# Optimization experiments

Hardware: AMD Instinct MI355X
Metric: run time of the kernel (lower is better)

The kernel has to match this reference:

```python
import jax, jax.numpy as jnp
import numpy as np

V = 50000
E = 800000
B, CIN, COUT, K = 4, 64, 128, 4


def setup_inputs() -> dict:
    key = jax.random.key(0)
    k1, k2, k3, k4, k5 = jax.random.split(key, 5)
    x = jax.random.normal(k1, (B, CIN, V), dtype=jnp.float32)
    lap_rows = jnp.sort(jax.random.randint(k2, (E,), 0, V, dtype=jnp.int32))
    lap_cols = jax.random.randint(k3, (E,), 0, V, dtype=jnp.int32)
    # scale ~1/sqrt(avg_degree) so recurrence stays bounded (laplacian-like spectrum)
    lap_vals = jax.random.normal(k4, (E,), dtype=jnp.float32) * (1.0 / np.sqrt(16.0))
    # kaiming init per module: std = sqrt(2/(Cin*K))
    weight = jax.random.normal(k5, (K, CIN, COUT), dtype=jnp.float32) * np.sqrt(2.0 / (CIN * K))
    bias = jnp.full((COUT,), 0.01, dtype=jnp.float32)
    return {"x": x, "lap_rows": lap_rows, "lap_cols": lap_cols,
            "lap_vals": lap_vals, "weight": weight, "bias": bias}


def reference(x, lap_rows, lap_cols, lap_vals, weight, bias):
    # x: (B, Cin, V); laplacian sparse COO (rows, cols, vals); weight: (K, Cin, Cout)
    Bn, Cin, Vn = x.shape
    Kn = weight.shape[0]

    def spmm(z):  # z: (V, B*Cin) -> laplacian @ z
        return jax.ops.segment_sum(lap_vals[:, None] * z[lap_cols], lap_rows,
                                   num_segments=Vn)

    def contract(z, w):  # (V, B*Cin) x (Cin, Cout) -> (V, B, Cout)
        return jnp.einsum('vbi,io->vbo', z.reshape(Vn, Bn, Cin), w)

    x0 = jnp.transpose(x, (2, 0, 1)).reshape(Vn, Bn * Cin)
    # fused Chebyshev recurrence: accumulate weight contraction per step
    out = contract(x0, weight[0])
    if Kn > 1:
        x1 = spmm(x0)
        out = out + contract(x1, weight[1])
        for k in range(2, Kn):
            x2 = 2.0 * spmm(x1) - x0
            out = out + contract(x2, weight[k])
            x0, x1 = x1, x2
    out = out + bias  # broadcast over (V, B, Cout)
    return jnp.transpose(out, (1, 2, 0))  # (B, Cout, V)
```

## Files before the change

kernel.cpp:

```cpp
#include <hip/hip_runtime.h>
#include <hip/hip_bf16.h>

#define VN 50000
#define EN 800000
#define BN 4
#define CINN 64
#define COUTN 128
#define KN 4
#define FN 256

typedef __attribute__((ext_vector_type(8))) short short8;
typedef __attribute__((ext_vector_type(8))) unsigned short ushort8;
typedef __attribute__((ext_vector_type(4))) float floatx4;

__device__ __forceinline__ float bf2f(unsigned short u) {
    union { unsigned int i; float f; } c;
    c.i = ((unsigned int)u) << 16;
    return c.f;
}
__device__ __forceinline__ unsigned short f2bf(float f) {
    __hip_bfloat16 h = __float2bfloat16(f);
    return *reinterpret_cast<unsigned short*>(&h);
}

#define RP_BLOCKS 196
#define WT_BLOCKS 128
#define EP_BLOCKS 3125
#define TP_BX 782
#define TP_BLOCKS (TP_BX * 4)

__global__ __launch_bounds__(256) void setup_fused(const int* __restrict__ rows,
                                                   int* __restrict__ row_ptr,
                                                   const float* __restrict__ w,
                                                   ushort* __restrict__ wT,
                                                   const float* __restrict__ x,
                                                   ushort* __restrict__ x0,
                                                   const int* __restrict__ cols,
                                                   const float* __restrict__ vals,
                                                   unsigned long long* __restrict__ epack) {
    __shared__ float tile[64][65];
    int blk = blockIdx.x;
    int tid = threadIdx.x;
    if (blk < RP_BLOCKS) {
        int v = blk * 256 + tid;
        if (v > VN) return;
        int lo = 0, hi = EN;
        while (lo < hi) {
            int mid = (lo + hi) >> 1;
            if (rows[mid] < v) lo = mid + 1; else hi = mid;
        }
        row_ptr[v] = lo;
        return;
    }
    if (blk < RP_BLOCKS + WT_BLOCKS) {
        int idx = (blk - RP_BLOCKS) * 256 + tid;
        int o = idx >> 8;
        int kk = idx & 255;
        wT[idx] = f2bf(w[(size_t)kk * COUTN + o]);
        return;
    }
    if (blk < RP_BLOCKS + WT_BLOCKS + EP_BLOCKS) {
        int idx = (blk - RP_BLOCKS - WT_BLOCKS) * 256 + tid;
        unsigned int c = (unsigned int)cols[idx];
        unsigned int wv = __float_as_uint(vals[idx]);
        epack[idx] = ((unsigned long long)wv << 32) | (unsigned long long)c;
        return;
    }
    int t = blk - RP_BLOCKS - WT_BLOCKS - EP_BLOCKS;
    int v0 = (t % TP_BX) * 64;
    int f0 = (t / TP_BX) * 64;
    int tx = tid & 63;
    int ty = tid >> 6;
#pragma unroll
    for (int r = 0; r < 16; ++r) {
        int f = f0 + ty + r * 4;
        int v = v0 + tx;
        if (v < VN) tile[ty + r * 4][tx] = x[(size_t)f * VN + v];
    }
    __syncthreads();
#pragma unroll
    for (int r = 0; r < 16; ++r) {
        int v = v0 + ty + r * 4;
        int f = f0 + tx;
        if (v < VN) x0[(size_t)v * FN + f] = f2bf(tile[tx][ty + r * 4]);
    }
}

__global__ __launch_bounds__(256) void spmm_cheb_bf16(ushort* __restrict__ out,
                                                      const ushort* __restrict__ z,
                                                      const ushort* __restrict__ prev,
                                                      const int* __restrict__ row_ptr,
                                                      const unsigned long long* __restrict__ epack,
                                                      float alpha, float beta) {
    int row = (int)((blockIdx.x * blockDim.x + threadIdx.x) >> 6);
    int lane = threadIdx.x & 63;
    if (row >= VN) return;
    int e0 = row_ptr[row];
    int e1 = row_ptr[row + 1];
    int half = lane >> 5;
    int fl = (lane & 31) * 8;

    float acc0[8], acc1[8];
#pragma unroll
    for (int j = 0; j < 8; ++j) { acc0[j] = 0.f; acc1[j] = 0.f; }

    int e = e0 + half;
    for (; e + 6 < e1; e += 8) {
        unsigned long long d0 = epack[e];
        unsigned long long d1 = epack[e + 2];
        unsigned long long d2 = epack[e + 4];
        unsigned long long d3 = epack[e + 6];
        ushort8 z0 = *reinterpret_cast<const ushort8*>(z + (size_t)(unsigned int)d0 * FN + fl);
        ushort8 z1 = *reinterpret_cast<const ushort8*>(z + (size_t)(unsigned int)d1 * FN + fl);
        ushort8 z2 = *reinterpret_cast<const ushort8*>(z + (size_t)(unsigned int)d2 * FN + fl);
        ushort8 z3 = *reinterpret_cast<const ushort8*>(z + (size_t)(unsigned int)d3 * FN + fl);
        float w0 = __uint_as_float((unsigned int)(d0 >> 32));
        float w1 = __uint_as_float((unsigned int)(d1 >> 32));
        float w2 = __uint_as_float((unsigned int)(d2 >> 32));
        float w3 = __uint_as_float((unsigned int)(d3 >> 32));
#pragma unroll
        for (int j = 0; j < 8; ++j) acc0[j] += w0 * bf2f(z0[j]);
#pragma unroll
        for (int j = 0; j < 8; ++j) acc1[j] += w1 * bf2f(z1[j]);
#pragma unroll
        for (int j = 0; j < 8; ++j) acc0[j] += w2 * bf2f(z2[j]);
#pragma unroll
        for (int j = 0; j < 8; ++j) acc1[j] += w3 * bf2f(z3[j]);
    }
    for (; e + 2 < e1; e += 4) {
        unsigned long long d0 = epack[e];
        unsigned long long d1 = epack[e + 2];
        ushort8 z0 = *reinterpret_cast<const ushort8*>(z + (size_t)(unsigned int)d0 * FN + fl);
        ushort8 z1 = *reinterpret_cast<const ushort8*>(z + (size_t)(unsigned int)d1 * FN + fl);
        float w0 = __uint_as_float((unsigned int)(d0 >> 32));
        float w1 = __uint_as_float((unsigned int)(d1 >> 32));
#pragma unroll
        for (int j = 0; j < 8; ++j) acc0[j] += w0 * bf2f(z0[j]);
#pragma unroll
        for (int j = 0; j < 8; ++j) acc1[j] += w1 * bf2f(z1[j]);
    }
    for (; e < e1; e += 2) {
        unsigned long long d0 = epack[e];
        ushort8 z0 = *reinterpret_cast<const ushort8*>(z + (size_t)(unsigned int)d0 * FN + fl);
        float w0 = __uint_as_float((unsigned int)(d0 >> 32));
#pragma unroll
        for (int j = 0; j < 8; ++j) acc0[j] += w0 * bf2f(z0[j]);
    }
#pragma unroll
    for (int j = 0; j < 8; ++j) acc0[j] += acc1[j];
#pragma unroll
    for (int j = 0; j < 8; ++j) acc0[j] += __shfl(acc0[j], lane ^ 32);

    if (half == 0) {
        ushort8 res;
        if (beta != 0.f) {
            ushort8 pv = *reinterpret_cast<const ushort8*>(prev + (size_t)row * FN + fl);
#pragma unroll
            for (int j = 0; j < 8; ++j)
                res[j] = f2bf(alpha * acc0[j] + beta * bf2f(pv[j]));
        } else {
#pragma unroll
            for (int j = 0; j < 8; ++j)
                res[j] = f2bf(alpha * acc0[j]);
        }
        *reinterpret_cast<ushort8*>(out + (size_t)row * FN + fl) = res;
    }
}

__global__ __launch_bounds__(256) void cheb_gemm_mfma(float* __restrict__ out,
                                                      const ushort* __restrict__ xbase,
                                                      const ushort* __restrict__ wT,
                                                      const float* __restrict__ bias) {
    __shared__ __align__(16) short lsA[128 * 64];
    __shared__ __align__(16) short lsB[128 * 64];

    int b = blockIdx.y;
    int v0 = blockIdx.x * 128;
    int tid = threadIdx.x;
    int lane = tid & 63;
    int w = tid >> 6;
    int mw = w & 1;
    int nw = w >> 1;
    int ln = lane & 15;
    int quad = lane >> 4;

    int srow = tid >> 1;
    int posBase = (tid & 1) * 4;

    floatx4 acc[4][4];
#pragma unroll
    for (int mi = 0; mi < 4; ++mi)
#pragma unroll
        for (int ni = 0; ni < 4; ++ni) acc[mi][ni] = (floatx4){0.f, 0.f, 0.f, 0.f};

    for (int kc = 0; kc < 4; ++kc) {
        __syncthreads();
#pragma unroll
        for (int j = 0; j < 4; ++j) {
            int pos = posBase + j;
            int g = pos ^ (srow & 7);
            uint4 val = *reinterpret_cast<const uint4*>(wT + (size_t)srow * 256 + kc * 64 + g * 8);
            *reinterpret_cast<uint4*>(&lsA[(srow * 8 + pos) * 8]) = val;
        }
        {
            const ushort* xk = xbase + (size_t)kc * VN * FN;
            int v = v0 + srow;
            bool ok = (v < VN);
            const ushort* src = xk + (size_t)v * FN + b * CINN;
#pragma unroll
            for (int j = 0; j < 4; ++j) {
                int pos = posBase + j;
                int g = pos ^ (srow & 7);
                uint4 val;
                if (ok) val = *reinterpret_cast<const uint4*>(src + g * 8);
                else    val = make_uint4(0u, 0u, 0u, 0u);
                *reinterpret_cast<uint4*>(&lsB[(srow * 8 + pos) * 8]) = val;
            }
        }
        __syncthreads();

#pragma unroll
        for (int s = 0; s < 2; ++s) {
            short8 afr[4], bfr[4];
#pragma unroll
            for (int mi = 0; mi < 4; ++mi) {
                int r = mw * 64 + mi * 16 + ln;
                int pos = (s * 4 + quad) ^ (r & 7);
                afr[mi] = *reinterpret_cast<const short8*>(&lsA[(r * 8 + pos) * 8]);
            }
#pragma unroll
            for (int ni = 0; ni < 4; ++ni) {
                int r = nw * 64 + ni * 16 + ln;
                int pos = (s * 4 + quad) ^ (r & 7);
                bfr[ni] = *reinterpret_cast<const short8*>(&lsB[(r * 8 + pos) * 8]);
            }
#pragma unroll
            for (int mi = 0; mi < 4; ++mi)
#pragma unroll
                for (int ni = 0; ni < 4; ++ni)
                    acc[mi][ni] = __builtin_amdgcn_mfma_f32_16x16x32_bf16(
                        afr[mi], bfr[ni], acc[mi][ni], 0, 0, 0);
        }
    }

#pragma unroll
    for (int mi = 0; mi < 4; ++mi) {
#pragma unroll
        for (int r = 0; r < 4; ++r) {
            int o = mw * 64 + mi * 16 + quad * 4 + r;
            float bv = bias[o];
            size_t obase = (size_t)(b * COUTN + o) * VN;
#pragma unroll
            for (int ni = 0; ni < 4; ++ni) {
                int v = v0 + nw * 64 + ni * 16 + ln;
                if (v < VN) out[obase + v] = acc[mi][ni][r] + bv;
            }
        }
    }
}

extern "C" void kernel_launch(void* const* d_in, const int* in_sizes, int n_in,
                              void* d_out, int out_size, void* d_ws, size_t ws_size,
                              hipStream_t stream) {
    const float* x        = (const float*)d_in[0];
    const int*   lap_rows = (const int*)d_in[1];
    const int*   lap_cols = (const int*)d_in[2];
    const float* lap_vals = (const float*)d_in[3];
    const float* weight   = (const float*)d_in[4];
    const float* bias     = (const float*)d_in[5];
    float* out = (float*)d_out;

    char* ws = (char*)d_ws;
    ushort* x0 = (ushort*)ws;
    ushort* x1 = x0 + (size_t)VN * FN;
    ushort* x2 = x1 + (size_t)VN * FN;
    ushort* x3 = x2 + (size_t)VN * FN;
    size_t xbytes = (size_t)4 * VN * FN * sizeof(ushort);
    int* row_ptr = (int*)(ws + xbytes);
    size_t rp_end = xbytes + (size_t)(VN + 1) * sizeof(int);
    rp_end = (rp_end + 15) & ~(size_t)15;
    ushort* wT = (ushort*)(ws + rp_end);
    size_t wt_end = rp_end + (size_t)COUTN * FN * sizeof(ushort);
    unsigned long long* epack = (unsigned long long*)(ws + wt_end);

    setup_fused<<<RP_BLOCKS + WT_BLOCKS + EP_BLOCKS + TP_BLOCKS, 256, 0, stream>>>(
        lap_rows, row_ptr, weight, wT, x, x0, lap_cols, lap_vals, epack);
    spmm_cheb_bf16<<<(VN + 3) / 4, 256, 0, stream>>>(x1, x0, x0, row_ptr, epack, 1.f, 0.f);
    spmm_cheb_bf16<<<(VN + 3) / 4, 256, 0, stream>>>(x2, x1, x0, row_ptr, epack, 2.f, -1.f);
    spmm_cheb_bf16<<<(VN + 3) / 4, 256, 0, stream>>>(x3, x2, x1, row_ptr, epack, 2.f, -1.f);
    cheb_gemm_mfma<<<dim3((VN + 127) / 128, BN), 256, 0, stream>>>(out, x0, wT, bias);
}
```

Measured before the change: 374.8 us.

## Packed-FMA SpMM accumulation and retiled, prefetched GEMM with vectorized stores

The SpMM inner loops now accumulate in float2 vectors so the compiler can emit packed FMA instructions. The GEMM is retiled to 64 vertices per block, and its operands are swapped so the output fragments run along the vertex dimension. That lets each thread write four contiguous floats per store, and the block now prefetches the next k-chunk into registers before the current chunk's MFMAs run. The aim is lower ALU cost in SpMM and more occupancy, latency hiding and coalesced stores in the GEMM, at the price of more blocks and more loads of the weight tile.

```diff
diff --git a/kernel.cpp b/kernel.cpp
--- a/kernel.cpp
+++ b/kernel.cpp
@@ -12,6 +12,7 @@
 typedef __attribute__((ext_vector_type(8))) short short8;
 typedef __attribute__((ext_vector_type(8))) unsigned short ushort8;
 typedef __attribute__((ext_vector_type(4))) float floatx4;
+typedef __attribute__((ext_vector_type(2))) float floatx2;
 
 __device__ __forceinline__ float bf2f(unsigned short u) {
     union { unsigned int i; float f; } c;
@@ -100,9 +101,11 @@
     int half = lane >> 5;
     int fl = (lane & 31) * 8;
 
-    float acc0[8], acc1[8];
-#pragma unroll
-    for (int j = 0; j < 8; ++j) { acc0[j] = 0.f; acc1[j] = 0.f; }
+    floatx2 A0[4], A1[4];
+#pragma unroll
+    for (int p = 0; p < 4; ++p) { A0[p] = (floatx2){0.f, 0.f}; A1[p] = (floatx2){0.f, 0.f}; }
+
+#define ZPAIR(zz, p) ((floatx2){bf2f((zz)[2*(p)]), bf2f((zz)[2*(p)+1])})
 
     int e = e0 + half;
     for (; e + 6 < e1; e += 8) {
@@ -118,14 +121,16 @@
         float w1 = __uint_as_float((unsigned int)(d1 >> 32));
         float w2 = __uint_as_float((unsigned int)(d2 >> 32));
         float w3 = __uint_as_float((unsigned int)(d3 >> 32));
-#pragma unroll
-        for (int j = 0; j < 8; ++j) acc0[j] += w0 * bf2f(z0[j]);
-#pragma unroll
-        for (int j = 0; j < 8; ++j) acc1[j] += w1 * bf2f(z1[j]);
-#pragma unroll
-        for (int j = 0; j < 8; ++j) acc0[j] += w2 * bf2f(z2[j]);
-#pragma unroll
-        for (int j = 0; j < 8; ++j) acc1[j] += w3 * bf2f(z3[j]);
+        floatx2 wv0 = (floatx2){w0, w0}, wv1 = (floatx2){w1, w1};
+        floatx2 wv2 = (floatx2){w2, w2}, wv3 = (floatx2){w3, w3};
+#pragma unroll
+        for (int p = 0; p < 4; ++p) A0[p] += wv0 * ZPAIR(z0, p);
+#pragma unroll
+        for (int p = 0; p < 4; ++p) A1[p] += wv1 * ZPAIR(z1, p);
+#pragma unroll
+        for (int p = 0; p < 4; ++p) A0[p] += wv2 * ZPAIR(z2, p);
+#pragma unroll
+        for (int p = 0; p < 4; ++p) A1[p] += wv3 * ZPAIR(z3, p);
     }
     for (; e + 2 < e1; e += 4) {
         unsigned long long d0 = epack[e];
@@ -134,20 +139,29 @@
         ushort8 z1 = *reinterpret_cast<const ushort8*>(z + (size_t)(unsigned int)d1 * FN + fl);
         float w0 = __uint_as_float((unsigned int)(d0 >> 32));
         float w1 = __uint_as_float((unsigned int)(d1 >> 32));
-#pragma unroll
-        for (int j = 0; j < 8; ++j) acc0[j] += w0 * bf2f(z0[j]);
-#pragma unroll
-        for (int j = 0; j < 8; ++j) acc1[j] += w1 * bf2f(z1[j]);
+        floatx2 wv0 = (floatx2){w0, w0}, wv1 = (floatx2){w1, w1};
+#pragma unroll
+        for (int p = 0; p < 4; ++p) A0[p] += wv0 * ZPAIR(z0, p);
+#pragma unroll
+        for (int p = 0; p < 4; ++p) A1[p] += wv1 * ZPAIR(z1, p);
     }
     for (; e < e1; e += 2) {
         unsigned long long d0 = epack[e];
         ushort8 z0 = *reinterpret_cast<const ushort8*>(z + (size_t)(unsigned int)d0 * FN + fl);
         float w0 = __uint_as_float((unsigned int)(d0 >> 32));
-#pragma unroll
-        for (int j = 0; j < 8; ++j) acc0[j] += w0 * bf2f(z0[j]);
-    }
-#pragma unroll
-    for (int j = 0; j < 8; ++j) acc0[j] += acc1[j];
+        floatx2 wv0 = (floatx2){w0, w0};
+#pragma unroll
+        for (int p = 0; p < 4; ++p) A0[p] += wv0 * ZPAIR(z0, p);
+    }
+#undef ZPAIR
+
+    float acc0[8];
+#pragma unroll
+    for (int p = 0; p < 4; ++p) {
+        floatx2 m = A0[p] + A1[p];
+        acc0[2 * p] = m[0];
+        acc0[2 * p + 1] = m[1];
+    }
 #pragma unroll
     for (int j = 0; j < 8; ++j) acc0[j] += __shfl(acc0[j], lane ^ 32);
 
@@ -167,93 +181,117 @@
     }
 }
 
-__global__ __launch_bounds__(256) void cheb_gemm_mfma(float* __restrict__ out,
-                                                      const ushort* __restrict__ xbase,
-                                                      const ushort* __restrict__ wT,
-                                                      const float* __restrict__ bias) {
-    __shared__ __align__(16) short lsA[128 * 64];
-    __shared__ __align__(16) short lsB[128 * 64];
+__global__ __launch_bounds__(256, 4) void cheb_gemm_mfma(float* __restrict__ out,
+                                                         const ushort* __restrict__ xbase,
+                                                         const ushort* __restrict__ wT,
+                                                         const float* __restrict__ bias) {
+    __shared__ __align__(16) short lsX[64 * 64];
+    __shared__ __align__(16) short lsW[128 * 64];
 
     int b = blockIdx.y;
-    int v0 = blockIdx.x * 128;
+    int v0 = blockIdx.x * 64;
     int tid = threadIdx.x;
     int lane = tid & 63;
     int w = tid >> 6;
-    int mw = w & 1;
-    int nw = w >> 1;
+    int wv = w & 1;
+    int wo = w >> 1;
     int ln = lane & 15;
     int quad = lane >> 4;
 
-    int srow = tid >> 1;
-    int posBase = (tid & 1) * 4;
-
-    floatx4 acc[4][4];
-#pragma unroll
-    for (int mi = 0; mi < 4; ++mi)
+    int srowW = tid >> 1;
+    int posW0 = (tid & 1) * 4;
+    int srowX = tid >> 2;
+    int posX0 = (tid & 3) * 2;
+    int vX = v0 + srowX;
+    bool okX = (vX < VN);
+
+    floatx4 acc[2][4];
+#pragma unroll
+    for (int mi = 0; mi < 2; ++mi)
 #pragma unroll
         for (int ni = 0; ni < 4; ++ni) acc[mi][ni] = (floatx4){0.f, 0.f, 0.f, 0.f};
 
+    uint4 pW[4], pX[2];
+
+#define LOADW(KC)                                                                       \
+    {                                                                                   \
+        _Pragma("unroll")                                                               \
+        for (int j = 0; j < 4; ++j) {                                                   \
+            int g = (posW0 + j) ^ (srowW & 7);                                          \
+            pW[j] = *reinterpret_cast<const uint4*>(wT + (size_t)srowW * 256 + (KC) * 64 + g * 8); \
+        }                                                                               \
+    }
+#define LOADX(KC)                                                                       \
+    {                                                                                   \
+        const ushort* src = xbase + (size_t)(KC) * VN * FN + (size_t)vX * FN + b * CINN; \
+        _Pragma("unroll")                                                               \
+        for (int j = 0; j < 2; ++j) {                                                   \
+            int g = (posX0 + j) ^ (srowX & 7);                                          \
+            if (okX) pX[j] = *reinterpret_cast<const uint4*>(src + g * 8);              \
+            else     pX[j] = make_uint4(0u, 0u, 0u, 0u);                                \
+        }                                                                               \
+    }
+
+    LOADW(0);
+    LOADX(0);
+
+#pragma unroll
     for (int kc = 0; kc < 4; ++kc) {
         __syncthreads();
 #pragma unroll
-        for (int j = 0; j < 4; ++j) {
-            int pos = posBase + j;
-            int g = pos ^ (srow & 7);
-            uint4 val = *reinterpret_cast<const uint4*>(wT + (size_t)srow * 256 + kc * 64 + g * 8);
-            *reinterpret_cast<uint4*>(&lsA[(srow * 8 + pos) * 8]) = val;
-        }
-        {
-            const ushort* xk = xbase + (size_t)kc * VN * FN;
-            int v = v0 + srow;
-            bool ok = (v < VN);
-            const ushort* src = xk + (size_t)v * FN + b * CINN;
-#pragma unroll
-            for (int j = 0; j < 4; ++j) {
-                int pos = posBase + j;
-                int g = pos ^ (srow & 7);
-                uint4 val;
-                if (ok) val = *reinterpret_cast<const uint4*>(src + g * 8);
-                else    val = make_uint4(0u, 0u, 0u, 0u);
-                *reinterpret_cast<uint4*>(&lsB[(srow * 8 + pos) * 8]) = val;
+        for (int j = 0; j < 4; ++j)
+            *reinterpret_cast<uint4*>(&lsW[(srowW * 8 + posW0 + j) * 8]) = pW[j];
+#pragma unroll
+        for (int j = 0; j < 2; ++j)
+            *reinterpret_cast<uint4*>(&lsX[(srowX * 8 + posX0 + j) * 8]) = pX[j];
+        __syncthreads();
+
+        if (kc < 3) {
+            LOADW(kc + 1);
+            LOADX(kc + 1);
+        }
+
+#pragma unroll
+        for (int s = 0; s < 2; ++s) {
+            short8 afr[2], bfr[4];
+#pragma unroll
+            for (int mi = 0; mi < 2; ++mi) {
+                int r = wv * 32 + mi * 16 + ln;
+                int pos = (s * 4 + quad) ^ (r & 7);
+                afr[mi] = *reinterpret_cast<const short8*>(&lsX[(r * 8 + pos) * 8]);
             }
-        }
-        __syncthreads();
-
-#pragma unroll
-        for (int s = 0; s < 2; ++s) {
-            short8 afr[4], bfr[4];
-#pragma unroll
-            for (int mi = 0; mi < 4; ++mi) {
-                int r = mw * 64 + mi * 16 + ln;
+#pragma unroll
+            for (int ni = 0; ni < 4; ++ni) {
+                int r = wo * 64 + ni * 16 + ln;
                 int pos = (s * 4 + quad) ^ (r & 7);
-                afr[mi] = *reinterpret_cast<const short8*>(&lsA[(r * 8 + pos) * 8]);
+                bfr[ni] = *reinterpret_cast<const short8*>(&lsW[(r * 8 + pos) * 8]);
             }
 #pragma unroll
-            for (int ni = 0; ni < 4; ++ni) {
-                int r = nw * 64 + ni * 16 + ln;
-                int pos = (s * 4 + quad) ^ (r & 7);
-                bfr[ni] = *reinterpret_cast<const short8*>(&lsB[(r * 8 + pos) * 8]);
-            }
-#pragma unroll
-            for (int mi = 0; mi < 4; ++mi)
+            for (int mi = 0; mi < 2; ++mi)
 #pragma unroll
                 for (int ni = 0; ni < 4; ++ni)
                     acc[mi][ni] = __builtin_amdgcn_mfma_f32_16x16x32_bf16(
                         afr[mi], bfr[ni], acc[mi][ni], 0, 0, 0);
         }
     }
-
-#pragma unroll
-    for (int mi = 0; mi < 4; ++mi) {
-#pragma unroll
-        for (int r = 0; r < 4; ++r) {
-            int o = mw * 64 + mi * 16 + quad * 4 + r;
+#undef LOADW
+#undef LOADX
+
+#pragma unroll
+    for (int mi = 0; mi < 2; ++mi) {
+        int vb = v0 + wv * 32 + mi * 16 + quad * 4;
+#pragma unroll
+        for (int ni = 0; ni < 4; ++ni) {
+            int o = wo * 64 + ni * 16 + ln;
             float bv = bias[o];
             size_t obase = (size_t)(b * COUTN + o) * VN;
-#pragma unroll
-            for (int ni = 0; ni < 4; ++ni) {
-                int v = v0 + nw * 64 + ni * 16 + ln;
-                if (v < VN) out[obase + v] = acc[mi][ni][r] + bv;
+            floatx4 res = acc[mi][ni] + bv;
+            if (vb + 3 < VN) {
+                *reinterpret_cast<floatx4*>(out + obase + vb) = res;
+            } else {
+#pragma unroll
+                for (int r = 0; r < 4; ++r)
+                    if (vb + r < VN) out[obase + vb + r] = res[r];
             }
         }
     }
@@ -288,5 +326,5 @@
     spmm_cheb_bf16<<<(VN + 3) / 4, 256, 0, stream>>>(x1, x0, x0, row_ptr, epack, 1.f, 0.f);
     spmm_cheb_bf16<<<(VN + 3) / 4, 256, 0, stream>>>(x2, x1, x0, row_ptr, epack, 2.f, -1.f);
     spmm_cheb_bf16<<<(VN + 3) / 4, 256, 0, stream>>>(x3, x2, x1, row_ptr, epack, 2.f, -1.f);
-    cheb_gemm_mfma<<<dim3((VN + 127) / 128, BN), 256, 0, stream>>>(out, x0, wT, bias);
-}
+    cheb_gemm_mfma<<<dim3((VN + 63) / 64, BN), 256, 0, stream>>>(out, x0, wT, bias);
+}
```

Measured after the change: 421.8 us. 12.5% more time.

## Double-buffer GEMM LDS tiles using direct global-to-LDS async loads

Applied to the files above, without the earlier changes.

Rewrites the Chebyshev GEMM staging so each chunk's weight and feature tiles are loaded with global_load_lds straight into LDS, skipping the trip through registers. Two LDS buffers let the next K-chunk's load overlap the current chunk's MFMA work, with one barrier per iteration instead of two. This doubles LDS use per block to 64KB, which may lower occupancy. It also drops the row bounds check, so the last partial block reads past the valid vertex rows.

```diff
diff --git a/kernel.cpp b/kernel.cpp
--- a/kernel.cpp
+++ b/kernel.cpp
@@ -21,6 +21,12 @@
 __device__ __forceinline__ unsigned short f2bf(float f) {
     __hip_bfloat16 h = __float2bfloat16(f);
     return *reinterpret_cast<unsigned short*>(&h);
+}
+
+typedef __attribute__((address_space(1))) const unsigned int guint;
+typedef __attribute__((address_space(3))) unsigned int luint;
+__device__ __forceinline__ void gload_lds16(const void* g, void* l) {
+    __builtin_amdgcn_global_load_lds((guint*)g, (luint*)l, 16, 0, 0);
 }
 
 #define RP_BLOCKS 196
@@ -171,8 +177,7 @@
                                                       const ushort* __restrict__ xbase,
                                                       const ushort* __restrict__ wT,
                                                       const float* __restrict__ bias) {
-    __shared__ __align__(16) short lsA[128 * 64];
-    __shared__ __align__(16) short lsB[128 * 64];
+    __shared__ __align__(16) short lds[2][16384];
 
     int b = blockIdx.y;
     int v0 = blockIdx.x * 128;
@@ -184,8 +189,8 @@
     int ln = lane & 15;
     int quad = lane >> 4;
 
-    int srow = tid >> 1;
-    int posBase = (tid & 1) * 4;
+    int lr = lane >> 3;
+    int lg = (lane & 7) ^ lr;
 
     floatx4 acc[4][4];
 #pragma unroll
@@ -193,31 +198,26 @@
 #pragma unroll
         for (int ni = 0; ni < 4; ++ni) acc[mi][ni] = (floatx4){0.f, 0.f, 0.f, 0.f};
 
+#define STAGE(BUF, KC)                                                              \
+    {                                                                               \
+        const ushort* xk = xbase + (size_t)(KC) * VN * FN;                          \
+        _Pragma("unroll")                                                           \
+        for (int j = 0; j < 4; ++j) {                                               \
+            int c = w * 4 + j;                                                      \
+            int r = c * 8 + lr;                                                     \
+            gload_lds16(wT + (size_t)r * 256 + (KC) * 64 + lg * 8,                  \
+                        &lds[BUF][c * 512]);                                        \
+            gload_lds16(xk + (size_t)(v0 + r) * FN + b * CINN + lg * 8,             \
+                        &lds[BUF][8192 + c * 512]);                                 \
+        }                                                                           \
+    }
+
+    int cur = 0;
+    STAGE(0, 0);
+    __syncthreads();
+
     for (int kc = 0; kc < 4; ++kc) {
-        __syncthreads();
-#pragma unroll
-        for (int j = 0; j < 4; ++j) {
-            int pos = posBase + j;
-            int g = pos ^ (srow & 7);
-            uint4 val = *reinterpret_cast<const uint4*>(wT + (size_t)srow * 256 + kc * 64 + g * 8);
-            *reinterpret_cast<uint4*>(&lsA[(srow * 8 + pos) * 8]) = val;
-        }
-        {
-            const ushort* xk = xbase + (size_t)kc * VN * FN;
-            int v = v0 + srow;
-            bool ok = (v < VN);
-            const ushort* src = xk + (size_t)v * FN + b * CINN;
-#pragma unroll
-            for (int j = 0; j < 4; ++j) {
-                int pos = posBase + j;
-                int g = pos ^ (srow & 7);
-                uint4 val;
-                if (ok) val = *reinterpret_cast<const uint4*>(src + g * 8);
-                else    val = make_uint4(0u, 0u, 0u, 0u);
-                *reinterpret_cast<uint4*>(&lsB[(srow * 8 + pos) * 8]) = val;
-            }
-        }
-        __syncthreads();
+        if (kc < 3) STAGE(cur ^ 1, kc + 1);
 
 #pragma unroll
         for (int s = 0; s < 2; ++s) {
@@ -226,13 +226,13 @@
             for (int mi = 0; mi < 4; ++mi) {
                 int r = mw * 64 + mi * 16 + ln;
                 int pos = (s * 4 + quad) ^ (r & 7);
-                afr[mi] = *reinterpret_cast<const short8*>(&lsA[(r * 8 + pos) * 8]);
+                afr[mi] = *reinterpret_cast<const short8*>(&lds[cur][(r * 8 + pos) * 8]);
             }
 #pragma unroll
             for (int ni = 0; ni < 4; ++ni) {
                 int r = nw * 64 + ni * 16 + ln;
                 int pos = (s * 4 + quad) ^ (r & 7);
-                bfr[ni] = *reinterpret_cast<const short8*>(&lsB[(r * 8 + pos) * 8]);
+                bfr[ni] = *reinterpret_cast<const short8*>(&lds[cur][8192 + (r * 8 + pos) * 8]);
             }
 #pragma unroll
             for (int mi = 0; mi < 4; ++mi)
@@ -241,7 +241,10 @@
                     acc[mi][ni] = __builtin_amdgcn_mfma_f32_16x16x32_bf16(
                         afr[mi], bfr[ni], acc[mi][ni], 0, 0, 0);
         }
-    }
+        __syncthreads();
+        cur ^= 1;
+    }
+#undef STAGE
 
 #pragma unroll
     for (int mi = 0; mi < 4; ++mi) {
```

Measured after the change: 378.7 us. Within noise of the previous version (+1.0%).
